# Kernel optimization log

Measured on AMD Instinct MI355X. Metric: run time of the kernel, lower is better.

Reference implementation:

```python
import jax, jax.numpy as jnp
import numpy as np

B, C, IMG, P = 64, 3, 224, 16
D, L, H, DH, M, NC = 768, 12, 12, 64, 3072, 1000
INNER = H * DH
PD = C * P * P          # patch_dim = 768
NP = (IMG // P) ** 2    # 196 patches


def setup_inputs() -> dict:
    key = jax.random.key(0)
    ks = jax.random.split(key, 16)
    s = 0.02
    nrm = lambda k, shape: jax.random.normal(k, shape, jnp.float32) * s
    return dict(
        img=jax.random.normal(ks[0], (B, C, IMG, IMG), jnp.float32),
        patch_ln1_g=jnp.ones(PD), patch_ln1_b=jnp.zeros(PD),
        patch_w=nrm(ks[1], (PD, D)), patch_b=jnp.zeros(D),
        patch_ln2_g=jnp.ones(D), patch_ln2_b=jnp.zeros(D),
        pos_emb=nrm(ks[2], (1, NP + 1, D)),
        cls_tok=nrm(ks[3], (1, 1, D)),
        attn_ln_g=jnp.ones((L, D)), attn_ln_b=jnp.zeros((L, D)),
        w_qkv=nrm(ks[4], (L, D, 3 * INNER)),
        w_out=nrm(ks[5], (L, INNER, D)), b_out=jnp.zeros((L, D)),
        ff_ln_g=jnp.ones((L, D)), ff_ln_b=jnp.zeros((L, D)),
        ff_w1=nrm(ks[6], (L, D, M)), ff_b1=jnp.zeros((L, M)),
        ff_w2=nrm(ks[7], (L, M, D)), ff_b2=jnp.zeros((L, D)),
        final_ln_g=jnp.ones(D), final_ln_b=jnp.zeros(D),
        head_w=nrm(ks[8], (D, NC)), head_b=jnp.zeros(NC),
    )


def _ln(x, g, b, eps=1e-5):
    m = x.mean(-1, keepdims=True)
    v = ((x - m) ** 2).mean(-1, keepdims=True)
    return (x - m) / jnp.sqrt(v + eps) * g + b


def reference(img, patch_ln1_g, patch_ln1_b, patch_w, patch_b, patch_ln2_g,
              patch_ln2_b, pos_emb, cls_tok, attn_ln_g, attn_ln_b, w_qkv,
              w_out, b_out, ff_ln_g, ff_ln_b, ff_w1, ff_b1, ff_w2, ff_b2,
              final_ln_g, final_ln_b, head_w, head_b):
    b, c, hh, ww = img.shape
    h, w = hh // P, ww // P
    # Rearrange 'b c (h p1) (w p2) -> b (h w) (p1 p2 c)'
    x = img.reshape(b, c, h, P, w, P).transpose(0, 2, 4, 3, 5, 1).reshape(b, h * w, P * P * c)
    x = _ln(x, patch_ln1_g, patch_ln1_b)
    x = x @ patch_w + patch_b
    x = _ln(x, patch_ln2_g, patch_ln2_b)
    n = x.shape[1]
    x = jnp.concatenate([jnp.broadcast_to(cls_tok, (b, 1, x.shape[-1])), x], axis=1)
    x = x + pos_emb[:, : n + 1]
    scale = DH ** -0.5
    for l in range(L):
        xn = _ln(x, attn_ln_g[l], attn_ln_b[l])
        qkv = xn @ w_qkv[l]  # [b, n+1, 3*inner]
        q, k, v = jnp.split(qkv, 3, axis=-1)
        sp = lambda t: t.reshape(b, -1, H, DH).transpose(0, 2, 1, 3)  # b h n d
        q, k, v = sp(q), sp(k), sp(v)
        # softmax variant: exp(scores*scale), normalize by sum + eps (no max-subtract, faithful to source)
        numer = jnp.exp(jnp.einsum('bhid,bhjd->bhij', q, k) * scale)
        attn = numer / (numer.sum(-1, keepdims=True) + 1e-8)
        out = jnp.einsum('bhij,bhjd->bhid', attn, v)
        out = out.transpose(0, 2, 1, 3).reshape(b, -1, INNER)
        x = out @ w_out[l] + b_out[l] + x
        xn = _ln(x, ff_ln_g[l], ff_ln_b[l])
        hid = jax.nn.gelu(xn @ ff_w1[l] + ff_b1[l], approximate=False)
        x = hid @ ff_w2[l] + ff_b2[l] + x
    x = _ln(x, final_ln_g, final_ln_b)
    return x[:, 0] @ head_w + head_b
```

## Files before the change

### kernel.cpp

```cpp
#include <hip/hip_runtime.h>
#include <hip/hip_bf16.h>
#include <math.h>

#define B_     64
#define NTOK   197
#define NPATCH 196
#define D768   768
#define NL     12
#define NH     12
#define MFF    3072
#define NCLS   1000
#define ROWS   (B_ * NTOK)
#define PROWS  (B_ * NPATCH)
#define ROWS_PAD 12672

typedef unsigned short ushort;
typedef __bf16 bf16x8 __attribute__((ext_vector_type(8)));
typedef float  f32x4  __attribute__((ext_vector_type(4)));
typedef unsigned short u16x4 __attribute__((ext_vector_type(4)));

__device__ __forceinline__ ushort f2b(float f) {
  __hip_bfloat16 h = __float2bfloat16(f);
  return *reinterpret_cast<ushort*>(&h);
}
__device__ __forceinline__ float b2f(ushort u) {
  unsigned int v = ((unsigned int)u) << 16;
  float f;
  __builtin_memcpy(&f, &v, 4);
  return f;
}

__device__ __forceinline__ void gload16(const ushort* g, ushort* lds) {
  __builtin_amdgcn_global_load_lds((const __attribute__((address_space(1))) void*)g,
                                   (__attribute__((address_space(3))) void*)lds, 16, 0, 0);
}

__device__ __forceinline__ float gelu_f(float v) {
  float t = v * fmaf(0.0713548162726f, v * v, 1.5957691216f);
  return v / (1.0f + __expf(-t));
}

__device__ __forceinline__ void block_mean_rstd(float s, float sq, float& mean, float& rstd) {
#pragma unroll
  for (int off = 32; off; off >>= 1) { s += __shfl_xor(s, off); sq += __shfl_xor(sq, off); }
  __shared__ float ss[4], ssq[4];
  int w = threadIdx.x >> 6;
  if ((threadIdx.x & 63) == 0) { ss[w] = s; ssq[w] = sq; }
  __syncthreads();
  s  = ss[0] + ss[1] + ss[2] + ss[3];
  sq = ssq[0] + ssq[1] + ssq[2] + ssq[3];
  mean = s * (1.0f / 768.0f);
  float var = sq * (1.0f / 768.0f) - mean * mean;
  rstd = rsqrtf(var + 1e-5f);
}

__global__ __launch_bounds__(256) void ln_rows_b(const ushort* __restrict__ in, long in_stride,
                                                 const float* __restrict__ g,
                                                 const float* __restrict__ bta,
                                                 ushort* __restrict__ out) {
  const ushort* xr = in + (size_t)blockIdx.x * in_stride;
  int t = threadIdx.x;
  float v0 = b2f(xr[t]), v1 = b2f(xr[t + 256]), v2 = b2f(xr[t + 512]);
  float mean, rstd;
  block_mean_rstd(v0 + v1 + v2, v0 * v0 + v1 * v1 + v2 * v2, mean, rstd);
  ushort* o = out + (size_t)blockIdx.x * 768;
  o[t]       = f2b((v0 - mean) * rstd * g[t]       + bta[t]);
  o[t + 256] = f2b((v1 - mean) * rstd * g[t + 256] + bta[t + 256]);
  o[t + 512] = f2b((v2 - mean) * rstd * g[t + 512] + bta[t + 512]);
}

__global__ __launch_bounds__(256) void patch_ln1(const float* __restrict__ img,
                                                 const float* __restrict__ g,
                                                 const float* __restrict__ bta,
                                                 ushort* __restrict__ xp) {
  int pidx = blockIdx.x;
  int b = pidx / NPATCH, hw = pidx % NPATCH;
  int ph = hw / 14, pw = hw % 14;
  int t = threadIdx.x;
  float v[3];
#pragma unroll
  for (int u = 0; u < 3; ++u) {
    int k = t + u * 256;
    int c = k % 3, p2 = (k / 3) & 15, p1 = k / 48;
    v[u] = img[(((size_t)b * 3 + c) * 224 + ph * 16 + p1) * 224 + pw * 16 + p2];
  }
  float mean, rstd;
  block_mean_rstd(v[0] + v[1] + v[2], v[0] * v[0] + v[1] * v[1] + v[2] * v[2], mean, rstd);
  ushort* o = xp + (size_t)pidx * 768;
#pragma unroll
  for (int u = 0; u < 3; ++u) { int k = t + u * 256; o[k] = f2b((v[u] - mean) * rstd * g[k] + bta[k]); }
}

__global__ __launch_bounds__(256) void ln2_pos(const float* __restrict__ xe,
                                               const float* __restrict__ g,
                                               const float* __restrict__ bta,
                                               const float* __restrict__ pos,
                                               ushort* __restrict__ x) {
  int pidx = blockIdx.x;
  int b = pidx / NPATCH, i = pidx % NPATCH;
  const float* xr = xe + (size_t)pidx * 768;
  int t = threadIdx.x;
  float v0 = xr[t], v1 = xr[t + 256], v2 = xr[t + 512];
  float mean, rstd;
  block_mean_rstd(v0 + v1 + v2, v0 * v0 + v1 * v1 + v2 * v2, mean, rstd);
  const float* p = pos + (size_t)(1 + i) * 768;
  ushort* o = x + ((size_t)b * NTOK + 1 + i) * 768;
  o[t]       = f2b((v0 - mean) * rstd * g[t]       + bta[t]       + p[t]);
  o[t + 256] = f2b((v1 - mean) * rstd * g[t + 256] + bta[t + 256] + p[t + 256]);
  o[t + 512] = f2b((v2 - mean) * rstd * g[t + 512] + bta[t + 512] + p[t + 512]);
}

__global__ __launch_bounds__(256) void cls_init(const float* __restrict__ cls_tok,
                                                const float* __restrict__ pos,
                                                ushort* __restrict__ x) {
  int b = blockIdx.x, t = threadIdx.x;
  ushort* o = x + (size_t)b * NTOK * 768;
#pragma unroll
  for (int u = 0; u < 3; ++u) { int k = t + u * 256; o[k] = f2b(cls_tok[k] + pos[k]); }
}

__global__ __launch_bounds__(256) void transpose_cast(const float* __restrict__ W,
                                                      ushort* __restrict__ Wt,
                                                      int K, int N) {
  __shared__ float t[32][33];
  int n0 = blockIdx.x * 32, k0 = blockIdx.y * 32;
  int tx = threadIdx.x, ty = threadIdx.y;
#pragma unroll
  for (int u = 0; u < 32; u += 8) {
    int n = n0 + tx;
    t[ty + u][tx] = (n < N) ? W[(size_t)(k0 + ty + u) * N + n] : 0.f;
  }
  __syncthreads();
#pragma unroll
  for (int u = 0; u < 32; u += 8) {
    int n = n0 + ty + u;
    if (n < N) Wt[(size_t)n * K + k0 + tx] = f2b(t[tx][ty + u]);
  }
}

__device__ __forceinline__ void transpose_layer(int bid,
                                                const float* wq, const float* wo,
                                                const float* w1, const float* w2,
                                                ushort* tq, ushort* to,
                                                ushort* t1, ushort* t2) {
  const float* W; ushort* Wt; int K, N, xt;
  if (bid < 1728)      {             W = wq; Wt = tq; K = 768;  N = 2304; xt = 72; }
  else if (bid < 2304) { bid -= 1728; W = wo; Wt = to; K = 768;  N = 768;  xt = 24; }
  else if (bid < 4608) { bid -= 2304; W = w1; Wt = t1; K = 768;  N = 3072; xt = 96; }
  else                 { bid -= 4608; W = w2; Wt = t2; K = 3072; N = 768;  xt = 24; }
  int n0 = (bid % xt) * 32, k0 = (bid / xt) * 32;
  __shared__ float t[32][33];
  int tx = threadIdx.x, ty = threadIdx.y;
#pragma unroll
  for (int u = 0; u < 32; u += 8)
    t[ty + u][tx] = W[(size_t)(k0 + ty + u) * N + n0 + tx];
  __syncthreads();
#pragma unroll
  for (int u = 0; u < 32; u += 8)
    Wt[(size_t)(n0 + ty + u) * K + k0 + tx] = f2b(t[tx][ty + u]);
}

__global__ __launch_bounds__(256) void transpose4(const float* __restrict__ wq,
                                                  const float* __restrict__ wo,
                                                  const float* __restrict__ w1,
                                                  const float* __restrict__ w2,
                                                  ushort* __restrict__ tq,
                                                  ushort* __restrict__ to,
                                                  ushort* __restrict__ t1,
                                                  ushort* __restrict__ t2) {
  transpose_layer(blockIdx.x, wq, wo, w1, w2, tq, to, t1, t2);
}

__global__ __launch_bounds__(256) void transpose_all(const float* __restrict__ wq,
                                                     const float* __restrict__ wo,
                                                     const float* __restrict__ w1,
                                                     const float* __restrict__ w2,
                                                     ushort* __restrict__ tq,
                                                     ushort* __restrict__ to,
                                                     ushort* __restrict__ t1,
                                                     ushort* __restrict__ t2) {
  int l = blockIdx.x / 6912, bid = blockIdx.x % 6912;
  transpose_layer(bid,
                  wq + (size_t)l * 768 * 2304, wo + (size_t)l * 768 * 768,
                  w1 + (size_t)l * 768 * MFF,  w2 + (size_t)l * MFF * 768,
                  tq + (size_t)l * 2304 * 768, to + (size_t)l * 768 * 768,
                  t1 + (size_t)l * MFF * 768,  t2 + (size_t)l * 768 * MFF);
}

template<int EP, int RESID, int OBF>
__global__ __launch_bounds__(256, 4) void gemm_v6(const ushort* __restrict__ A,
                                                  const ushort* __restrict__ Bt,
                                                  const float* __restrict__ bias,
                                                  const void* __restrict__ resid,
                                                  void* __restrict__ Cv,
                                                  int M, int N, int K) {
  __shared__ ushort smem[2 * 8192];

  const int tid = threadIdx.x;
  const int w = tid >> 6, l = tid & 63;
  const int fr = l & 15, fc = l >> 4;

  const int ntx = gridDim.x;
  const int nwg = ntx * gridDim.y;
  const int orig = blockIdx.y * ntx + blockIdx.x;
  const int q = nwg >> 3, r = nwg & 7, xcd = orig & 7, idx = orig >> 3;
  const int wg = (xcd < r ? xcd * (q + 1) : r * (q + 1) + (xcd - r) * q) + idx;
  const int row0 = (wg / ntx) * 128, col0 = (wg % ntx) * 128;

  const int wr = (w >> 1) * 64, wc = (w & 1) * 64;

  const int srow = tid >> 2;
  const int sg = (tid & 3) ^ ((srow >> 1) & 3);
  const ushort* pA0 = A  + (size_t)(row0 + srow) * K + sg * 8;
  const ushort* pA1 = A  + (size_t)(row0 + 64 + srow) * K + sg * 8;
  const ushort* pB0 = Bt + (size_t)(col0 + srow) * K + sg * 8;
  const ushort* pB1 = Bt + (size_t)(col0 + 64 + srow) * K + sg * 8;

  auto stage = [&](int t_, ushort* dst) {
    const int k0 = t_ * 32;
    gload16(pA0 + k0, dst + tid * 8);
    gload16(pA1 + k0, dst + (tid + 256) * 8);
    gload16(pB0 + k0, dst + 4096 + tid * 8);
    gload16(pB1 + k0, dst + 4096 + (tid + 256) * 8);
  };

  int idxA[4], idxB[4];
#pragma unroll
  for (int m = 0; m < 4; ++m) {
    int rA = wr + m * 16 + fr;
    idxA[m] = rA * 32 + ((fc ^ ((rA >> 1) & 3)) << 3);
  }
#pragma unroll
  for (int n = 0; n < 4; ++n) {
    int rB = wc + n * 16 + fr;
    idxB[n] = rB * 32 + ((fc ^ ((rB >> 1) & 3)) << 3);
  }

  f32x4 acc[4][4] = {};

  auto compute = [&](const ushort* As) {
    const ushort* Bs = As + 4096;
    bf16x8 a_[4], b_[4];
#pragma unroll
    for (int m = 0; m < 4; ++m) a_[m] = *(const bf16x8*)(As + idxA[m]);
#pragma unroll
    for (int n = 0; n < 4; ++n) b_[n] = *(const bf16x8*)(Bs + idxB[n]);
#pragma unroll
    for (int m = 0; m < 4; ++m)
#pragma unroll
      for (int n = 0; n < 4; ++n)
        acc[m][n] = __builtin_amdgcn_mfma_f32_16x16x32_bf16(b_[n], a_[m], acc[m][n], 0, 0, 0);
  };

#define VM4() asm volatile("s_waitcnt vmcnt(4)" ::: "memory")
#define VM0() asm volatile("s_waitcnt vmcnt(0)" ::: "memory")

  const int NT = K >> 5;

  stage(0, smem);
  for (int t = 0; t < NT; t += 2) {
    if (t + 1 < NT) { stage(t + 1, smem + 8192); VM4(); } else VM0();
    __builtin_amdgcn_s_barrier();
    compute(smem);
    __builtin_amdgcn_s_barrier();
    if (t + 1 < NT) {
      if (t + 2 < NT) { stage(t + 2, smem); VM4(); } else VM0();
      __builtin_amdgcn_s_barrier();
      compute(smem + 8192);
      __builtin_amdgcn_s_barrier();
    }
  }
#undef VM4
#undef VM0

  if (!OBF) {
    float* Cf = (float*)Cv;
#pragma unroll
    for (int m = 0; m < 4; ++m) {
      int row = row0 + wr + m * 16 + fr;
      if (row >= M) continue;
#pragma unroll
      for (int n = 0; n < 4; ++n) {
        int col = col0 + wc + n * 16 + fc * 4;
        f32x4 v = acc[m][n];
        if (bias) v += *(const f32x4*)(bias + col);
        if (EP) {
#pragma unroll
          for (int rr = 0; rr < 4; ++rr) v[rr] = gelu_f(v[rr]);
        }
        if (RESID) v += *(const f32x4*)((const float*)resid + (size_t)row * N + col);
        *(f32x4*)(Cf + (size_t)row * N + col) = v;
      }
    }
  } else {
    __syncthreads();
    ushort* Cw = smem + w * 4096;
#pragma unroll
    for (int m = 0; m < 4; ++m) {
      int rl = m * 16 + fr;
      int row = row0 + wr + rl;
#pragma unroll
      for (int n = 0; n < 4; ++n) {
        int col = col0 + wc + n * 16 + fc * 4;
        f32x4 v = acc[m][n];
        if (bias) v += *(const f32x4*)(bias + col);
        if (EP) {
#pragma unroll
          for (int rr = 0; rr < 4; ++rr) v[rr] = gelu_f(v[rr]);
        }
        if (RESID) {
          u16x4 rv = *(const u16x4*)((const ushort*)resid + (size_t)row * N + col);
#pragma unroll
          for (int rr = 0; rr < 4; ++rr) v[rr] += b2f(rv[rr]);
        }
        u16x4 pk = { f2b(v[0]), f2b(v[1]), f2b(v[2]), f2b(v[3]) };
        int s = (n * 4 + fc) ^ (rl & 7);
        *(u16x4*)(Cw + rl * 64 + s * 4) = pk;
      }
    }
    ushort* Cb = (ushort*)Cv;
#pragma unroll
    for (int pp = 0; pp < 16; ++pp) {
      int rl = pp * 4 + (l >> 4);
      int cs = l & 15;
      u16x4 pk = *(const u16x4*)(Cw + rl * 64 + ((cs ^ (rl & 7)) * 4));
      int row = row0 + wr + rl;
      if (row < M) *(u16x4*)(Cb + (size_t)row * N + col0 + wc + cs * 4) = pk;
    }
  }
}

template<int EP, int RESID, int OBF>
__global__ __launch_bounds__(256) void gemm_bt(const ushort* __restrict__ A,
                                               const ushort* __restrict__ Bt,
                                               const float* __restrict__ bias,
                                               const float* __restrict__ resid,
                                               void* __restrict__ C,
                                               int M, int N, int K) {
  __shared__ ushort As[128 * 32];
  __shared__ ushort Bs[128 * 32];
  int tid = threadIdx.x;
  int w = tid >> 6, l = tid & 63;
  int fr = l & 15, fc = l >> 4;
  int row0 = blockIdx.y * 128, col0 = blockIdx.x * 128;
  int wr = (w >> 1) * 64, wc = (w & 1) * 64;

  int srow0 = w * 32 + (l >> 2);
  int srow1 = srow0 + 16;
  int sc0 = (((l & 3) ^ ((srow0 >> 1) & 3)) << 3);
  int sc1 = (((l & 3) ^ ((srow1 >> 1) & 3)) << 3);
  const ushort* ga0 = A  + (size_t)(row0 + srow0) * K + sc0;
  const ushort* ga1 = A  + (size_t)(row0 + srow1) * K + sc1;
  const ushort* gb0 = Bt + (size_t)(col0 + srow0) * K + sc0;
  const ushort* gb1 = Bt + (size_t)(col0 + srow1) * K + sc1;

  int idxA[4], idxB[4];
#pragma unroll
  for (int m = 0; m < 4; ++m) {
    int rA = wr + m * 16 + fr;
    idxA[m] = rA * 32 + ((fc ^ ((rA >> 1) & 3)) << 3);
  }
#pragma unroll
  for (int n = 0; n < 4; ++n) {
    int rB = wc + n * 16 + fr;
    idxB[n] = rB * 32 + ((fc ^ ((rB >> 1) & 3)) << 3);
  }

  f32x4 acc[4][4] = {};

  for (int k0 = 0; k0 < K; k0 += 32) {
    gload16(ga0 + k0, &As[w * 1024]);
    gload16(ga1 + k0, &As[w * 1024 + 512]);
    gload16(gb0 + k0, &Bs[w * 1024]);
    gload16(gb1 + k0, &Bs[w * 1024 + 512]);
    __syncthreads();
    bf16x8 af[4], bfr[4];
#pragma unroll
    for (int m = 0; m < 4; ++m) af[m] = *(const bf16x8*)(As + idxA[m]);
#pragma unroll
    for (int n = 0; n < 4; ++n) bfr[n] = *(const bf16x8*)(Bs + idxB[n]);
#pragma unroll
    for (int m = 0; m < 4; ++m)
#pragma unroll
      for (int n = 0; n < 4; ++n)
        acc[m][n] = __builtin_amdgcn_mfma_f32_16x16x32_bf16(af[m], bfr[n], acc[m][n], 0, 0, 0);
    __syncthreads();
  }

#pragma unroll
  for (int n = 0; n < 4; ++n) {
    int col = col0 + wc + n * 16 + fr;
    if (col >= N) continue;
    float bv = bias ? bias[col] : 0.f;
#pragma unroll
    for (int m = 0; m < 4; ++m) {
#pragma unroll
      for (int rr = 0; rr < 4; ++rr) {
        int row = row0 + wr + m * 16 + fc * 4 + rr;
        if (row >= M) continue;
        float v = acc[m][n][rr] + bv;
        if (EP == 1) v = 0.5f * v * (1.0f + erff(v * 0.70710678118654752f));
        if (RESID) v += resid[(size_t)row * N + col];
        if (OBF) ((ushort*)C)[(size_t)row * N + col] = f2b(v);
        else     ((float*)C)[(size_t)row * N + col]  = v;
      }
    }
  }
}

__global__ __launch_bounds__(256) void attn_mfma(const ushort* __restrict__ qkv,
                                                 ushort* __restrict__ aout) {
  int bid = blockIdx.x;
  int qt = bid & 3;
  int h  = (bid >> 2) % NH;
  int b  = (bid >> 2) / NH;
  int tid = threadIdx.x, w = tid >> 6, l = tid & 63;
  int fr = l & 15, fc = l >> 4;

  __shared__ ushort Vt[64 * 64];
  __shared__ ushort Pl[4 * 16 * 64];

  const size_t brow = (size_t)b * NTOK;
  int q0 = qt * 64 + w * 16;

  bf16x8 qf[2];
  {
    const ushort* qp = qkv + (brow + q0 + fr) * 2304 + h * 64 + fc * 8;
    qf[0] = *(const bf16x8*)qp;
    qf[1] = *(const bf16x8*)(qp + 32);
  }
  float rs[4] = {0.f, 0.f, 0.f, 0.f};
  f32x4 oc[4] = {};

  for (int kt = 0; kt < 4; ++kt) {
    __syncthreads();
    {
      int key = tid >> 2, d0 = (tid & 3) * 16;
      int j = kt * 64 + key;
      bool valid = j < NTOK;
      const ushort* vp = qkv + (brow + j) * 2304 + 1536 + h * 64 + d0;
      ushort vbuf[16];
      if (valid) {
        *(bf16x8*)(vbuf)     = *(const bf16x8*)vp;
        *(bf16x8*)(vbuf + 8) = *(const bf16x8*)(vp + 8);
      } else {
#pragma unroll
        for (int i = 0; i < 16; ++i) vbuf[i] = 0;
      }
#pragma unroll
      for (int i = 0; i < 16; ++i) {
        int d = d0 + i;
        int byte = d * 128 + ((((key >> 3)) ^ (d & 7)) << 4) + (key & 7) * 2;
        Vt[byte >> 1] = vbuf[i];
      }
    }
    f32x4 sc[4];
#pragma unroll
    for (int n = 0; n < 4; ++n) {
      f32x4 z = {};
      const ushort* kp = qkv + (brow + kt * 64 + n * 16 + fr) * 2304 + 768 + h * 64 + fc * 8;
      bf16x8 k0 = *(const bf16x8*)kp;
      bf16x8 k1 = *(const bf16x8*)(kp + 32);
      z = __builtin_amdgcn_mfma_f32_16x16x32_bf16(qf[0], k0, z, 0, 0, 0);
      z = __builtin_amdgcn_mfma_f32_16x16x32_bf16(qf[1], k1, z, 0, 0, 0);
      sc[n] = z;
    }
    float part[4] = {0.f, 0.f, 0.f, 0.f};
#pragma unroll
    for (int n = 0; n < 4; ++n) {
      int j = kt * 64 + n * 16 + fr;
      bool jv = j < NTOK;
#pragma unroll
      for (int rr = 0; rr < 4; ++rr) {
        float e = jv ? __expf(sc[n][rr] * 0.125f) : 0.f;
        part[rr] += e;
        int row = fc * 4 + rr, col = n * 16 + fr;
        int byte = row * 128 + (((col >> 3) ^ (row & 7)) << 4) + (col & 7) * 2;
        Pl[w * 1024 + (byte >> 1)] = f2b(e);
      }
    }
#pragma unroll
    for (int rr = 0; rr < 4; ++rr) {
      float p = part[rr];
      p += __shfl_xor(p, 1); p += __shfl_xor(p, 2);
      p += __shfl_xor(p, 4); p += __shfl_xor(p, 8);
      rs[rr] += p;
    }
    __syncthreads();
#pragma unroll
    for (int ks = 0; ks < 2; ++ks) {
      int prow = fr;
      int pbyte = prow * 128 + (((ks * 4 + fc) ^ (prow & 7)) << 4);
      bf16x8 pf = *(const bf16x8*)(Pl + w * 1024 + (pbyte >> 1));
#pragma unroll
      for (int n = 0; n < 4; ++n) {
        int d = n * 16 + fr;
        int vb = d * 128 + (((ks * 4 + fc) ^ (d & 7)) << 4);
        bf16x8 vf = *(const bf16x8*)(Vt + (vb >> 1));
        oc[n] = __builtin_amdgcn_mfma_f32_16x16x32_bf16(pf, vf, oc[n], 0, 0, 0);
      }
    }
  }
#pragma unroll
  for (int n = 0; n < 4; ++n) {
#pragma unroll
    for (int rr = 0; rr < 4; ++rr) {
      int qq = q0 + fc * 4 + rr;
      if (qq < NTOK) {
        float v = oc[n][rr] / (rs[rr] + 1e-8f);
        aout[(brow + qq) * 768 + h * 64 + n * 16 + fr] = f2b(v);
      }
    }
  }
}

extern "C" void kernel_launch(void* const* d_in, const int* in_sizes, int n_in,
                              void* d_out, int out_size, void* d_ws, size_t ws_size,
                              hipStream_t stream) {
  const float* img       = (const float*)d_in[0];
  const float* p_ln1_g   = (const float*)d_in[1];
  const float* p_ln1_b   = (const float*)d_in[2];
  const float* patch_w   = (const float*)d_in[3];
  const float* patch_b   = (const float*)d_in[4];
  const float* p_ln2_g   = (const float*)d_in[5];
  const float* p_ln2_b   = (const float*)d_in[6];
  const float* pos_emb   = (const float*)d_in[7];
  const float* cls_tok   = (const float*)d_in[8];
  const float* attn_ln_g = (const float*)d_in[9];
  const float* attn_ln_b = (const float*)d_in[10];
  const float* w_qkv     = (const float*)d_in[11];
  const float* w_out     = (const float*)d_in[12];
  const float* b_out     = (const float*)d_in[13];
  const float* ff_ln_g   = (const float*)d_in[14];
  const float* ff_ln_b   = (const float*)d_in[15];
  const float* ff_w1     = (const float*)d_in[16];
  const float* ff_b1     = (const float*)d_in[17];
  const float* ff_w2     = (const float*)d_in[18];
  const float* ff_b2     = (const float*)d_in[19];
  const float* fin_ln_g  = (const float*)d_in[20];
  const float* fin_ln_b  = (const float*)d_in[21];
  const float* head_w    = (const float*)d_in[22];
  const float* head_b    = (const float*)d_in[23];
  float* out = (float*)d_out;

  char* p = (char*)d_ws;
  auto alloc = [&](size_t bytes) { char* r = p; p += (bytes + 255) & ~(size_t)255; return r; };
  ushort* x      = (ushort*)alloc((size_t)ROWS_PAD * 768 * 2);
  ushort* xnb    = (ushort*)alloc((size_t)ROWS_PAD * 768 * 2);
  ushort* qkvb   = (ushort*)alloc((size_t)ROWS_PAD * 2304 * 2);
  ushort* aoutb  = (ushort*)alloc((size_t)ROWS_PAD * 768 * 2);
  ushort* pwt    = (ushort*)alloc((size_t)768 * 768 * 2);
  ushort* hwt    = (ushort*)alloc((size_t)1024 * 768 * 2);
  ushort* xclsb  = (ushort*)alloc((size_t)128 * 768 * 2);
  ushort* hidb   = qkvb;
  ushort* xpb    = xnb;
  float*  xe     = (float*)qkvb;

  const size_t SQ = (size_t)2304 * 768, SO = (size_t)768 * 768, S1 = (size_t)MFF * 768;
  size_t used = (size_t)(p - (char*)d_ws);
  bool oneshot = (used + 12 * (SQ + SO + 2 * S1) * 2 + 4096) <= ws_size;
  int nw = oneshot ? 12 : 1;
  ushort* wtq = (ushort*)alloc(nw * SQ * 2);
  ushort* wto = (ushort*)alloc(nw * SO * 2);
  ushort* wt1 = (ushort*)alloc(nw * S1 * 2);
  ushort* wt2 = (ushort*)alloc(nw * S1 * 2);

  dim3 blk(256), tblk(32, 8);

  transpose_cast<<<dim3(24, 24), tblk, 0, stream>>>(patch_w, pwt, 768, 768);
  transpose_cast<<<dim3(32, 24), tblk, 0, stream>>>(head_w, hwt, 768, 1000);
  if (oneshot)
    transpose_all<<<12 * 6912, tblk, 0, stream>>>(w_qkv, w_out, ff_w1, ff_w2,
                                                  wtq, wto, wt1, wt2);
  patch_ln1<<<PROWS, blk, 0, stream>>>(img, p_ln1_g, p_ln1_b, xpb);
  gemm_v6<0, 0, 0><<<dim3(6, 98), blk, 0, stream>>>(xpb, pwt, patch_b, nullptr, xe,
                                                    PROWS, 768, 768);
  ln2_pos<<<PROWS, blk, 0, stream>>>(xe, p_ln2_g, p_ln2_b, pos_emb, x);
  cls_init<<<B_, blk, 0, stream>>>(cls_tok, pos_emb, x);

  for (int l = 0; l < NL; ++l) {
    ushort* tq = wtq + (oneshot ? (size_t)l * SQ : 0);
    ushort* to = wto + (oneshot ? (size_t)l * SO : 0);
    ushort* t1 = wt1 + (oneshot ? (size_t)l * S1 : 0);
    ushort* t2 = wt2 + (oneshot ? (size_t)l * S1 : 0);
    if (!oneshot)
      transpose4<<<6912, tblk, 0, stream>>>(w_qkv + (size_t)l * 768 * 2304,
                                            w_out + (size_t)l * 768 * 768,
                                            ff_w1 + (size_t)l * 768 * MFF,
                                            ff_w2 + (size_t)l * MFF * 768,
                                            tq, to, t1, t2);

    ln_rows_b<<<ROWS, blk, 0, stream>>>(x, 768, attn_ln_g + (size_t)l * 768,
                                        attn_ln_b + (size_t)l * 768, xnb);
    gemm_v6<0, 0, 1><<<dim3(18, 99), blk, 0, stream>>>(xnb, tq, nullptr, nullptr, qkvb,
                                                       ROWS, 2304, 768);
    attn_mfma<<<B_ * NH * 4, blk, 0, stream>>>(qkvb, aoutb);
    gemm_v6<0, 1, 1><<<dim3(6, 99), blk, 0, stream>>>(aoutb, to, b_out + (size_t)l * 768,
                                                      x, x, ROWS, 768, 768);
    ln_rows_b<<<ROWS, blk, 0, stream>>>(x, 768, ff_ln_g + (size_t)l * 768,
                                        ff_ln_b + (size_t)l * 768, xnb);
    gemm_v6<1, 0, 1><<<dim3(24, 99), blk, 0, stream>>>(xnb, t1, ff_b1 + (size_t)l * MFF,
                                                       nullptr, hidb, ROWS, MFF, 768);
    gemm_v6<0, 1, 1><<<dim3(6, 99), blk, 0, stream>>>(hidb, t2, ff_b2 + (size_t)l * 768,
                                                      x, x, ROWS, 768, MFF);
  }

  ln_rows_b<<<B_, blk, 0, stream>>>(x, (long)NTOK * 768, fin_ln_g, fin_ln_b, xclsb);
  gemm_bt<0, 0, 0><<<dim3(8, 1), blk, 0, stream>>>(xclsb, hwt, head_b, nullptr, out,
                                                   B_, NCLS, 768);
}
```

Before: 4.228 ms.

## Add 128x256 GEMM tile for QKV/FF1, vectorize LayerNorm and weight transpose

Introduces gemm_v7, a 128x256 output tile GEMM with larger per-wave accumulators (4x8 MFMA fragments) and double-buffered LDS staging, used for the wide QKV and FF1 projections to raise operand reuse per loaded byte. LayerNorm rows now use 4-wide vector loads and stores on 192 threads, and the weight transpose-cast switches to 64x64 tiles with vectorized float4 reads and paired bf16 writes. The bigger tile halves the number of blocks and lowers occupancy (launch bounds 256,2), which could hurt latency hiding or leave CUs idle in the last wave.

```diff
diff --git a/kernel.cpp b/kernel.cpp
--- a/kernel.cpp
+++ b/kernel.cpp
@@ -18,6 +18,7 @@
 typedef __bf16 bf16x8 __attribute__((ext_vector_type(8)));
 typedef float  f32x4  __attribute__((ext_vector_type(4)));
 typedef unsigned short u16x4 __attribute__((ext_vector_type(4)));
+typedef unsigned short u16x2 __attribute__((ext_vector_type(2)));
 
 __device__ __forceinline__ ushort f2b(float f) {
   __hip_bfloat16 h = __float2bfloat16(f);
@@ -60,13 +61,23 @@
                                                  ushort* __restrict__ out) {
   const ushort* xr = in + (size_t)blockIdx.x * in_stride;
   int t = threadIdx.x;
-  float v0 = b2f(xr[t]), v1 = b2f(xr[t + 256]), v2 = b2f(xr[t + 512]);
+  float v0 = 0.f, v1 = 0.f, v2 = 0.f, v3 = 0.f;
+  if (t < 192) {
+    u16x4 xv = *(const u16x4*)(xr + t * 4);
+    v0 = b2f(xv[0]); v1 = b2f(xv[1]); v2 = b2f(xv[2]); v3 = b2f(xv[3]);
+  }
   float mean, rstd;
-  block_mean_rstd(v0 + v1 + v2, v0 * v0 + v1 * v1 + v2 * v2, mean, rstd);
-  ushort* o = out + (size_t)blockIdx.x * 768;
-  o[t]       = f2b((v0 - mean) * rstd * g[t]       + bta[t]);
-  o[t + 256] = f2b((v1 - mean) * rstd * g[t + 256] + bta[t + 256]);
-  o[t + 512] = f2b((v2 - mean) * rstd * g[t + 512] + bta[t + 512]);
+  block_mean_rstd(v0 + v1 + v2 + v3,
+                  v0 * v0 + v1 * v1 + v2 * v2 + v3 * v3, mean, rstd);
+  if (t < 192) {
+    f32x4 gv = *(const f32x4*)(g + t * 4);
+    f32x4 bv = *(const f32x4*)(bta + t * 4);
+    u16x4 o = { f2b((v0 - mean) * rstd * gv[0] + bv[0]),
+                f2b((v1 - mean) * rstd * gv[1] + bv[1]),
+                f2b((v2 - mean) * rstd * gv[2] + bv[2]),
+                f2b((v3 - mean) * rstd * gv[3] + bv[3]) };
+    *(u16x4*)(out + (size_t)blockIdx.x * 768 + t * 4) = o;
+  }
 }
 
 __global__ __launch_bounds__(256) void patch_ln1(const float* __restrict__ img,
@@ -138,26 +149,35 @@
   }
 }
 
-__device__ __forceinline__ void transpose_layer(int bid,
-                                                const float* wq, const float* wo,
-                                                const float* w1, const float* w2,
-                                                ushort* tq, ushort* to,
-                                                ushort* t1, ushort* t2) {
+__device__ __forceinline__ void transpose_layer64(int bid,
+                                                  const float* wq, const float* wo,
+                                                  const float* w1, const float* w2,
+                                                  ushort* tq, ushort* to,
+                                                  ushort* t1, ushort* t2) {
   const float* W; ushort* Wt; int K, N, xt;
-  if (bid < 1728)      {             W = wq; Wt = tq; K = 768;  N = 2304; xt = 72; }
-  else if (bid < 2304) { bid -= 1728; W = wo; Wt = to; K = 768;  N = 768;  xt = 24; }
-  else if (bid < 4608) { bid -= 2304; W = w1; Wt = t1; K = 768;  N = 3072; xt = 96; }
-  else                 { bid -= 4608; W = w2; Wt = t2; K = 3072; N = 768;  xt = 24; }
-  int n0 = (bid % xt) * 32, k0 = (bid / xt) * 32;
-  __shared__ float t[32][33];
-  int tx = threadIdx.x, ty = threadIdx.y;
-#pragma unroll
-  for (int u = 0; u < 32; u += 8)
-    t[ty + u][tx] = W[(size_t)(k0 + ty + u) * N + n0 + tx];
+  if (bid < 432)       {             W = wq; Wt = tq; K = 768;  N = 2304; xt = 36; }
+  else if (bid < 576)  { bid -= 432; W = wo; Wt = to; K = 768;  N = 768;  xt = 12; }
+  else if (bid < 1152) { bid -= 576; W = w1; Wt = t1; K = 768;  N = 3072; xt = 48; }
+  else                 { bid -= 1152; W = w2; Wt = t2; K = 3072; N = 768; xt = 12; }
+  int n0 = (bid % xt) * 64, k0 = (bid / xt) * 64;
+  __shared__ float t[64][65];
+  int id = threadIdx.x;
+  int tx = id & 15, ty = id >> 4;
+#pragma unroll
+  for (int u = 0; u < 4; ++u) {
+    int k = ty + 16 * u;
+    f32x4 v = *(const f32x4*)(W + (size_t)(k0 + k) * N + n0 + tx * 4);
+    t[k][tx * 4 + 0] = v[0]; t[k][tx * 4 + 1] = v[1];
+    t[k][tx * 4 + 2] = v[2]; t[k][tx * 4 + 3] = v[3];
+  }
   __syncthreads();
-#pragma unroll
-  for (int u = 0; u < 32; u += 8)
-    Wt[(size_t)(n0 + ty + u) * K + k0 + tx] = f2b(t[tx][ty + u]);
+  int wx = id & 31, wy = id >> 5;
+#pragma unroll
+  for (int u = 0; u < 8; ++u) {
+    int n = wy + 8 * u;
+    u16x2 o = { f2b(t[wx * 2][n]), f2b(t[wx * 2 + 1][n]) };
+    *(u16x2*)(Wt + (size_t)(n0 + n) * K + k0 + wx * 2) = o;
+  }
 }
 
 __global__ __launch_bounds__(256) void transpose4(const float* __restrict__ wq,
@@ -168,7 +188,7 @@
                                                   ushort* __restrict__ to,
                                                   ushort* __restrict__ t1,
                                                   ushort* __restrict__ t2) {
-  transpose_layer(blockIdx.x, wq, wo, w1, w2, tq, to, t1, t2);
+  transpose_layer64(blockIdx.x, wq, wo, w1, w2, tq, to, t1, t2);
 }
 
 __global__ __launch_bounds__(256) void transpose_all(const float* __restrict__ wq,
@@ -179,12 +199,12 @@
                                                      ushort* __restrict__ to,
                                                      ushort* __restrict__ t1,
                                                      ushort* __restrict__ t2) {
-  int l = blockIdx.x / 6912, bid = blockIdx.x % 6912;
-  transpose_layer(bid,
-                  wq + (size_t)l * 768 * 2304, wo + (size_t)l * 768 * 768,
-                  w1 + (size_t)l * 768 * MFF,  w2 + (size_t)l * MFF * 768,
-                  tq + (size_t)l * 2304 * 768, to + (size_t)l * 768 * 768,
-                  t1 + (size_t)l * MFF * 768,  t2 + (size_t)l * 768 * MFF);
+  int l = blockIdx.x / 1728, bid = blockIdx.x % 1728;
+  transpose_layer64(bid,
+                    wq + (size_t)l * 768 * 2304, wo + (size_t)l * 768 * 768,
+                    w1 + (size_t)l * 768 * MFF,  w2 + (size_t)l * MFF * 768,
+                    tq + (size_t)l * 2304 * 768, to + (size_t)l * 768 * 768,
+                    t1 + (size_t)l * MFF * 768,  t2 + (size_t)l * 768 * MFF);
 }
 
 template<int EP, int RESID, int OBF>
@@ -326,6 +346,153 @@
       u16x4 pk = *(const u16x4*)(Cw + rl * 64 + ((cs ^ (rl & 7)) * 4));
       int row = row0 + wr + rl;
       if (row < M) *(u16x4*)(Cb + (size_t)row * N + col0 + wc + cs * 4) = pk;
+    }
+  }
+}
+
+template<int EP, int RESID, int OBF>
+__global__ __launch_bounds__(256, 2) void gemm_v7(const ushort* __restrict__ A,
+                                                  const ushort* __restrict__ Bt,
+                                                  const float* __restrict__ bias,
+                                                  const float* __restrict__ resid,
+                                                  void* __restrict__ Cv,
+                                                  int M, int N, int K) {
+  __shared__ ushort smem[2 * 12288];
+
+  const int tid = threadIdx.x;
+  const int w = tid >> 6, l = tid & 63;
+  const int fr = l & 15, fc = l >> 4;
+
+  const int ntx = gridDim.x;
+  const int nwg = ntx * gridDim.y;
+  const int orig = blockIdx.y * ntx + blockIdx.x;
+  const int q = nwg >> 3, r = nwg & 7, xcd = orig & 7, idx = orig >> 3;
+  const int wg = (xcd < r ? xcd * (q + 1) : r * (q + 1) + (xcd - r) * q) + idx;
+  const int row0 = (wg / ntx) * 128, col0 = (wg % ntx) * 256;
+
+  const int wrow = (w >> 1) * 64, wcol = (w & 1) * 128;
+
+  const int srow = tid >> 2;
+  const int sg = (tid & 3) ^ ((srow >> 1) & 3);
+  const ushort* pA0 = A  + (size_t)(row0 + srow) * K + sg * 8;
+  const ushort* pA1 = A  + (size_t)(row0 + 64 + srow) * K + sg * 8;
+  const ushort* pB0 = Bt + (size_t)(col0 + srow) * K + sg * 8;
+  const ushort* pB1 = Bt + (size_t)(col0 + 64 + srow) * K + sg * 8;
+  const ushort* pB2 = Bt + (size_t)(col0 + 128 + srow) * K + sg * 8;
+  const ushort* pB3 = Bt + (size_t)(col0 + 192 + srow) * K + sg * 8;
+
+  auto stage = [&](int t_, ushort* dst) {
+    const int k0 = t_ * 32;
+    gload16(pA0 + k0, dst + tid * 8);
+    gload16(pA1 + k0, dst + (tid + 256) * 8);
+    ushort* db = dst + 4096;
+    gload16(pB0 + k0, db + tid * 8);
+    gload16(pB1 + k0, db + (tid + 256) * 8);
+    gload16(pB2 + k0, db + (tid + 512) * 8);
+    gload16(pB3 + k0, db + (tid + 768) * 8);
+  };
+
+  int idxA[4], idxB[8];
+#pragma unroll
+  for (int m = 0; m < 4; ++m) {
+    int rA = wrow + m * 16 + fr;
+    idxA[m] = rA * 32 + ((fc ^ ((rA >> 1) & 3)) << 3);
+  }
+#pragma unroll
+  for (int n = 0; n < 8; ++n) {
+    int rB = wcol + n * 16 + fr;
+    idxB[n] = rB * 32 + ((fc ^ ((rB >> 1) & 3)) << 3);
+  }
+
+  f32x4 acc[4][8] = {};
+
+  auto compute = [&](const ushort* As) {
+    const ushort* Bs = As + 4096;
+    bf16x8 a_[4], b_[8];
+#pragma unroll
+    for (int m = 0; m < 4; ++m) a_[m] = *(const bf16x8*)(As + idxA[m]);
+#pragma unroll
+    for (int n = 0; n < 8; ++n) b_[n] = *(const bf16x8*)(Bs + idxB[n]);
+#pragma unroll
+    for (int m = 0; m < 4; ++m)
+#pragma unroll
+      for (int n = 0; n < 8; ++n)
+        acc[m][n] = __builtin_amdgcn_mfma_f32_16x16x32_bf16(b_[n], a_[m], acc[m][n], 0, 0, 0);
+  };
+
+#define VM6() asm volatile("s_waitcnt vmcnt(6)" ::: "memory")
+#define VM0() asm volatile("s_waitcnt vmcnt(0)" ::: "memory")
+
+  const int NT = K >> 5;
+
+  stage(0, smem);
+  for (int t = 0; t < NT; t += 2) {
+    if (t + 1 < NT) { stage(t + 1, smem + 12288); VM6(); } else VM0();
+    __builtin_amdgcn_s_barrier();
+    compute(smem);
+    __builtin_amdgcn_s_barrier();
+    if (t + 1 < NT) {
+      if (t + 2 < NT) { stage(t + 2, smem); VM6(); } else VM0();
+      __builtin_amdgcn_s_barrier();
+      compute(smem + 12288);
+      __builtin_amdgcn_s_barrier();
+    }
+  }
+#undef VM6
+#undef VM0
+
+  if (!OBF) {
+    float* Cf = (float*)Cv;
+#pragma unroll
+    for (int m = 0; m < 4; ++m) {
+      int row = row0 + wrow + m * 16 + fr;
+      if (row >= M) continue;
+#pragma unroll
+      for (int n = 0; n < 8; ++n) {
+        int col = col0 + wcol + n * 16 + fc * 4;
+        f32x4 v = acc[m][n];
+        if (bias) v += *(const f32x4*)(bias + col);
+        if (EP) {
+#pragma unroll
+          for (int rr = 0; rr < 4; ++rr) v[rr] = gelu_f(v[rr]);
+        }
+        if (RESID) v += *(const f32x4*)(resid + (size_t)row * N + col);
+        *(f32x4*)(Cf + (size_t)row * N + col) = v;
+      }
+    }
+  } else {
+    ushort* Cw = smem + w * 4096;
+    ushort* Cb = (ushort*)Cv;
+#pragma unroll
+    for (int mp = 0; mp < 2; ++mp) {
+#pragma unroll
+      for (int m2 = 0; m2 < 2; ++m2) {
+        int m = mp * 2 + m2;
+        int rl = m2 * 16 + fr;
+#pragma unroll
+        for (int n = 0; n < 8; ++n) {
+          int col = col0 + wcol + n * 16 + fc * 4;
+          f32x4 v = acc[m][n];
+          if (bias) v += *(const f32x4*)(bias + col);
+          if (EP) {
+#pragma unroll
+            for (int rr = 0; rr < 4; ++rr) v[rr] = gelu_f(v[rr]);
+          }
+          u16x4 pk = { f2b(v[0]), f2b(v[1]), f2b(v[2]), f2b(v[3]) };
+          int s = (n * 4 + fc) ^ (rl & 7);
+          *(u16x4*)(Cw + rl * 128 + s * 4) = pk;
+        }
+      }
+      asm volatile("s_waitcnt lgkmcnt(0)" ::: "memory");
+#pragma unroll
+      for (int pp = 0; pp < 16; ++pp) {
+        int rl = pp * 2 + (l >> 5);
+        int cs = l & 31;
+        u16x4 pk = *(const u16x4*)(Cw + rl * 128 + ((cs ^ (rl & 7)) * 4));
+        int row = row0 + wrow + mp * 32 + rl;
+        if (row < M) *(u16x4*)(Cb + (size_t)row * N + col0 + wcol + cs * 4) = pk;
+      }
+      asm volatile("s_waitcnt lgkmcnt(0)" ::: "memory");
     }
   }
 }
@@ -570,8 +737,8 @@
   transpose_cast<<<dim3(24, 24), tblk, 0, stream>>>(patch_w, pwt, 768, 768);
   transpose_cast<<<dim3(32, 24), tblk, 0, stream>>>(head_w, hwt, 768, 1000);
   if (oneshot)
-    transpose_all<<<12 * 6912, tblk, 0, stream>>>(w_qkv, w_out, ff_w1, ff_w2,
-                                                  wtq, wto, wt1, wt2);
+    transpose_all<<<12 * 1728, blk, 0, stream>>>(w_qkv, w_out, ff_w1, ff_w2,
+                                                 wtq, wto, wt1, wt2);
   patch_ln1<<<PROWS, blk, 0, stream>>>(img, p_ln1_g, p_ln1_b, xpb);
   gemm_v6<0, 0, 0><<<dim3(6, 98), blk, 0, stream>>>(xpb, pwt, patch_b, nullptr, xe,
                                                     PROWS, 768, 768);
@@ -584,22 +751,22 @@
     ushort* t1 = wt1 + (oneshot ? (size_t)l * S1 : 0);
     ushort* t2 = wt2 + (oneshot ? (size_t)l * S1 : 0);
     if (!oneshot)
-      transpose4<<<6912, tblk, 0, stream>>>(w_qkv + (size_t)l * 768 * 2304,
-                                            w_out + (size_t)l * 768 * 768,
-                                            ff_w1 + (size_t)l * 768 * MFF,
-                                            ff_w2 + (size_t)l * MFF * 768,
-                                            tq, to, t1, t2);
+      transpose4<<<1728, blk, 0, stream>>>(w_qkv + (size_t)l * 768 * 2304,
+                                           w_out + (size_t)l * 768 * 768,
+                                           ff_w1 + (size_t)l * 768 * MFF,
+                                           ff_w2 + (size_t)l * MFF * 768,
+                                           tq, to, t1, t2);
 
     ln_rows_b<<<ROWS, blk, 0, stream>>>(x, 768, attn_ln_g + (size_t)l * 768,
                                         attn_ln_b + (size_t)l * 768, xnb);
-    gemm_v6<0, 0, 1><<<dim3(18, 99), blk, 0, stream>>>(xnb, tq, nullptr, nullptr, qkvb,
-                                                       ROWS, 2304, 768);
+    gemm_v7<0, 0, 1><<<dim3(9, 99), blk, 0, stream>>>(xnb, tq, nullptr, nullptr, qkvb,
+                                                      ROWS, 2304, 768);
     attn_mfma<<<B_ * NH * 4, blk, 0, stream>>>(qkvb, aoutb);
     gemm_v6<0, 1, 1><<<dim3(6, 99), blk, 0, stream>>>(aoutb, to, b_out + (size_t)l * 768,
                                                       x, x, ROWS, 768, 768);
     ln_rows_b<<<ROWS, blk, 0, stream>>>(x, 768, ff_ln_g + (size_t)l * 768,
                                         ff_ln_b + (size_t)l * 768, xnb);
-    gemm_v6<1, 0, 1><<<dim3(24, 99), blk, 0, stream>>>(xnb, t1, ff_b1 + (size_t)l * MFF,
+    gemm_v7<1, 0, 1><<<dim3(12, 99), blk, 0, stream>>>(xnb, t1, ff_b1 + (size_t)l * MFF,
                                                        nullptr, hidb, ROWS, MFF, 768);
     gemm_v6<0, 1, 1><<<dim3(6, 99), blk, 0, stream>>>(hidb, t2, ff_b2 + (size_t)l * 768,
                                                       x, x, ROWS, 768, MFF);
```

New measurement: 4.234 ms. Within noise of the previous version (+0.1%).
